# Kernel tuning notes

Hardware: AMD Instinct MI355X
Metric: run time of the kernel (lower is better)

Reference implementation:

```python
import jax, jax.numpy as jnp
import numpy as np
from functools import partial

H = 2048      # hidden_size
DI = 4096     # intermediate_size
N = 16        # ssm_state_size
K = 4         # conv_kernel_size
R = 128       # time_step_rank
B = 2
L = 1024


def setup_inputs() -> dict:
    key = jax.random.key(0)
    ks = jax.random.split(key, 10)
    s = 0.02
    return {
        "x": jax.random.normal(ks[0], (B, L, H), jnp.float32),
        "Win": jax.random.normal(ks[1], (2 * DI, H), jnp.float32) * s,      # in_proj weight
        "Wconv": jax.random.normal(ks[2], (DI, 1, K), jnp.float32) * 0.2,   # depthwise conv weight
        "bconv": jax.random.normal(ks[3], (DI,), jnp.float32) * 0.1,
        "Wx": jax.random.normal(ks[4], (R + 2 * N, DI), jnp.float32) * s,   # x_proj weight (no bias)
        "Wdt": jax.random.normal(ks[5], (DI, R), jnp.float32) * s,          # dt_proj weight
        "bdt": jax.random.normal(ks[6], (DI,), jnp.float32) * 0.1,
        "Wout": jax.random.normal(ks[7], (H, DI), jnp.float32) * s,         # out_proj weight (no bias)
        "A_log": jnp.log(jnp.broadcast_to(jnp.arange(1, N + 1, dtype=jnp.float32), (DI, N))),
        "D": jnp.ones((DI,), jnp.float32),
    }


def _silu(v):
    return v * jax.nn.sigmoid(v)


def _mamba_fwd(x, Win, Wconv, bconv, Wx, Wdt, bdt, Wout, A_log, D):
    sg = jax.lax.stop_gradient
    # in_proj -> [B, 2*DI, L]
    proj = jnp.einsum('blh,eh->bel', x, Win)
    hs, gate = proj[:, :DI], proj[:, DI:]          # [B, DI, L] each
    # depthwise causal conv1d, left pad K-1, trimmed to seq_len
    hs = jax.lax.conv_general_dilated(
        hs, Wconv, window_strides=(1,), padding=[(K - 1, 0)],
        dimension_numbers=('NCH', 'OIH', 'NCH'), feature_group_count=DI)
    hs = _silu(hs + bconv[None, :, None])          # [B, DI, L]
    # x_proj on [B, L, DI]
    ssm_p = jnp.einsum('bdl,pd->blp', hs, Wx)      # [B, L, R+2N]
    dt_in, Bm, Cm = ssm_p[..., :R], ssm_p[..., R:R + N], ssm_p[..., R + N:]
    dt = jax.nn.softplus(jnp.einsum('blr,dr->bld', dt_in, Wdt) + bdt)  # [B, L, DI]
    dt = jnp.transpose(dt, (0, 2, 1))              # [B, DI, L]
    A = -jnp.exp(A_log)                            # [DI, N]
    dA = jnp.exp(A[None, :, None, :] * dt[:, :, :, None])              # [B, DI, L, N]
    dBu = sg(dt[:, :, :, None] * Bm[:, None, :, :]) * hs[:, :, :, None]
    dA = sg(dA)
    Cm = sg(Cm)
    # sequential selective scan over time
    xs = (jnp.transpose(dA, (2, 0, 1, 3)),         # [L, B, DI, N]
          jnp.transpose(dBu, (2, 0, 1, 3)),
          jnp.transpose(Cm, (1, 0, 2)))            # [L, B, N]
    h0 = jnp.zeros((x.shape[0], DI, N), jnp.float32)

    def step(h, inp):
        dA_t, dBu_t, C_t = inp
        h = dA_t * h + dBu_t
        y = jnp.einsum('bdn,bn->bd', h, C_t)
        return h, y

    _, ys = jax.lax.scan(step, h0, xs)             # ys: [L, B, DI]
    y = jnp.transpose(ys, (1, 2, 0))               # [B, DI, L]
    y = y + hs * D[None, :, None]
    y = y * _silu(gate)
    y = y / 2.0 + sg(y / 2.0)                      # gradient-halving trick (fwd-identity)
    return jnp.einsum('bdl,hd->blh', y, Wout)      # [B, L, H]


def reference(x, Win, Wconv, bconv, Wx, Wdt, bdt, Wout, A_log, D):
    return _mamba_fwd(x, Win, Wconv, bconv, Wx, Wdt, bdt, Wout, A_log, D)
```

## Files before the change

kernel.cpp:

```cpp
#include <hip/hip_runtime.h>
#include <hip/hip_bf16.h>

#define HH 2048
#define DI 4096
#define NS 16
#define RR 128
#define NB 2
#define LL 1024
#define BL (NB*LL)
#define E2 (2*DI)
#define NPAD 256
#define NCOV 192
#define NC 16
#define CL (LL/NC)
#define KSPL 8

typedef __bf16  bf16x8 __attribute__((ext_vector_type(8)));
typedef unsigned short u16x8 __attribute__((ext_vector_type(8)));
typedef unsigned short u16x4 __attribute__((ext_vector_type(4)));
typedef float   f32x4  __attribute__((ext_vector_type(4)));
typedef _Float16 f16;
typedef _Float16 f16x4 __attribute__((ext_vector_type(4)));

__device__ __forceinline__ unsigned short f2bf(float f) {
  union { float f; unsigned u; } v; v.f = f;
  unsigned u = v.u;
  unsigned r = (u + 0x7FFFu + ((u >> 16) & 1u)) >> 16;
  return (unsigned short)r;
}
__device__ __forceinline__ float bf2f(unsigned short u) {
  union { unsigned u; float f; } v; v.u = ((unsigned)u) << 16; return v.f;
}

__device__ __forceinline__ float sigm(float x) { return 1.f / (1.f + __expf(-x)); }

__device__ __forceinline__ float softplus_hw(float v) {
  return (v > 20.f) ? v : __logf(1.f + __expf(v));
}

__device__ __forceinline__ void pow16(float q, float* w) {
  float q2 = q * q, q3 = q2 * q, q4 = q2 * q2;
  float q5 = q4 * q, q6 = q4 * q2, q7 = q4 * q3, q8 = q4 * q4;
  w[0]=q;    w[1]=q2;    w[2]=q3;    w[3]=q4;
  w[4]=q5;   w[5]=q6;    w[6]=q7;    w[7]=q8;
  w[8]=q8*q; w[9]=q8*q2; w[10]=q8*q3; w[11]=q8*q4;
  w[12]=q8*q5; w[13]=q8*q6; w[14]=q8*q7; w[15]=q8*q8;
}

__device__ __forceinline__ void gload_lds16(const void* g, void* l) {
  __builtin_amdgcn_global_load_lds(
      (const __attribute__((address_space(1))) void*)g,
      (__attribute__((address_space(3))) void*)l, 16, 0, 0);
}

#define CPRE_X    ((long)BL*HH/8)
#define CPRE_WIN  ((long)E2*HH/8)
#define CPRE_WX   ((long)NPAD*DI/8)
#define CPRE_WDT  ((long)DI*RR/8)
#define CPRE_WOUT ((long)HH*DI/8)
__global__ void cast_pre(const float* __restrict__ x, const float* __restrict__ Win,
                         const float* __restrict__ Wx, const float* __restrict__ Wdt,
                         const float* __restrict__ Wout,
                         unsigned short* __restrict__ xb, unsigned short* __restrict__ winb,
                         unsigned short* __restrict__ wxb, unsigned short* __restrict__ wdtb,
                         unsigned short* __restrict__ woutb) {
  const long NT = CPRE_X + CPRE_WIN + CPRE_WX + CPRE_WDT + CPRE_WOUT;
  long stride = (long)gridDim.x * blockDim.x;
  for (long c = (long)blockIdx.x * blockDim.x + threadIdx.x; c < NT; c += stride) {
    const float* src; unsigned short* dst; long i; bool zero = false;
    long c1 = c - CPRE_X, c2 = c1 - CPRE_WIN, c3 = c2 - CPRE_WX, c4 = c3 - CPRE_WDT;
    if (c < CPRE_X)        { src = x;    dst = xb;    i = c; }
    else if (c1 < CPRE_WIN){ src = Win;  dst = winb;  i = c1; }
    else if (c2 < CPRE_WX) { src = Wx;   dst = wxb;   i = c2; zero = (i >= 160L * (DI / 8)); }
    else if (c3 < CPRE_WDT){ src = Wdt;  dst = wdtb;  i = c3; }
    else                   { src = Wout; dst = woutb; i = c4; }
    u16x8 r;
    if (zero) {
      #pragma unroll
      for (int k = 0; k < 8; k++) r[k] = 0;
    } else {
      const float4* p = (const float4*)src + i * 2;
      float4 a = p[0], b = p[1];
      r[0]=f2bf(a.x); r[1]=f2bf(a.y); r[2]=f2bf(a.z); r[3]=f2bf(a.w);
      r[4]=f2bf(b.x); r[5]=f2bf(b.y); r[6]=f2bf(b.z); r[7]=f2bf(b.w);
    }
    ((u16x8*)dst)[i] = r;
  }
}

__global__ __launch_bounds__(256, 2) void gemm1_128(
    const unsigned short* __restrict__ A, const unsigned short* __restrict__ B,
    unsigned short* __restrict__ Chs, unsigned short* __restrict__ Cgate)
{
  __shared__ unsigned short As[128 * 32];
  __shared__ unsigned short Bs[128 * 32];

  const int tid  = threadIdx.x;
  const int lane = tid & 63;
  const int wid  = tid >> 6;
  const int mBlk = blockIdx.y * 128;
  const int nBlk = blockIdx.x * 128;
  const int wm = (wid >> 1) * 64;
  const int wn = (wid & 1) * 64;

  const int srow = wid * 32 + (lane >> 2);
  const int sk   = (lane & 3) * 8;
  const unsigned short* ga0 = A + (size_t)(mBlk + srow) * HH + sk;
  const unsigned short* ga1 = A + (size_t)(mBlk + srow + 16) * HH + sk;
  const unsigned short* gb0 = B + (size_t)(nBlk + srow) * HH + sk;
  const unsigned short* gb1 = B + (size_t)(nBlk + srow + 16) * HH + sk;
  unsigned short* la0 = &As[(wid * 32) * 32];
  unsigned short* la1 = &As[(wid * 32 + 16) * 32];
  unsigned short* lb0 = &Bs[(wid * 32) * 32];
  unsigned short* lb1 = &Bs[(wid * 32 + 16) * 32];

  const int fr = lane & 15;
  const int fq = lane >> 4;

  f32x4 acc[4][4];
  #pragma unroll
  for (int i = 0; i < 4; i++)
    #pragma unroll
    for (int j = 0; j < 4; j++) {
      acc[i][j][0] = 0.f; acc[i][j][1] = 0.f; acc[i][j][2] = 0.f; acc[i][j][3] = 0.f;
    }

  for (int k0 = 0; k0 < HH; k0 += 32) {
    __syncthreads();
    gload_lds16(ga0 + k0, la0);
    gload_lds16(ga1 + k0, la1);
    gload_lds16(gb0 + k0, lb0);
    gload_lds16(gb1 + k0, lb1);
    __syncthreads();
    bf16x8 af[4], bg[4];
    #pragma unroll
    for (int i = 0; i < 4; i++) {
      af[i] = *(const bf16x8*)&As[(wm + i * 16 + fr) * 32 + fq * 8];
      bg[i] = *(const bf16x8*)&Bs[(wn + i * 16 + fr) * 32 + fq * 8];
    }
    #pragma unroll
    for (int i = 0; i < 4; i++)
      #pragma unroll
      for (int j = 0; j < 4; j++)
        acc[i][j] = __builtin_amdgcn_mfma_f32_16x16x32_bf16(bg[j], af[i], acc[i][j], 0, 0, 0);
  }

  const int mr = lane & 15;
  const int nb = (lane >> 4) * 4;
  #pragma unroll
  for (int i = 0; i < 4; i++)
    #pragma unroll
    for (int j = 0; j < 4; j++) {
      int row = mBlk + wm + i * 16 + mr;
      int col = nBlk + wn + j * 16 + nb;
      u16x4 pk;
      #pragma unroll
      for (int r = 0; r < 4; r++) pk[r] = f2bf(acc[i][j][r]);
      if (nBlk < DI) *(u16x4*)&Chs[(size_t)row * DI + col] = pk;
      else           *(u16x4*)&Cgate[(size_t)row * DI + (col - DI)] = pk;
    }
}

__global__ __launch_bounds__(256, 2) void gemm2_splitk64(
    const unsigned short* __restrict__ A, const unsigned short* __restrict__ B,
    float* __restrict__ part)
{
  __shared__ unsigned short As[128 * 32];
  __shared__ unsigned short Bs[64 * 32];

  const int tid  = threadIdx.x;
  const int lane = tid & 63;
  const int wid  = tid >> 6;
  const int mBlk = blockIdx.y * 128;
  const int nBlk = blockIdx.x * 64;
  const int kBeg = blockIdx.z * (DI / KSPL);
  const int kEnd = kBeg + DI / KSPL;
  const int wm = (wid >> 1) * 64;
  const int wn = (wid & 1) * 32;

  const int srow = lane >> 2;
  const int sk   = (lane & 3) * 8;
  const unsigned short* ga0 = A + (size_t)(mBlk + wid * 32 + srow) * DI + sk;
  const unsigned short* ga1 = ga0 + (size_t)16 * DI;
  const unsigned short* gb  = B + (size_t)(nBlk + wid * 16 + srow) * DI + sk;
  unsigned short* la0 = &As[(wid * 32) * 32];
  unsigned short* la1 = &As[(wid * 32 + 16) * 32];
  unsigned short* lb  = &Bs[(wid * 16) * 32];

  const int fr = lane & 15;
  const int fq = lane >> 4;

  f32x4 acc[4][2];
  #pragma unroll
  for (int i = 0; i < 4; i++)
    #pragma unroll
    for (int j = 0; j < 2; j++) {
      acc[i][j][0] = 0.f; acc[i][j][1] = 0.f; acc[i][j][2] = 0.f; acc[i][j][3] = 0.f;
    }

  for (int k0 = kBeg; k0 < kEnd; k0 += 32) {
    __syncthreads();
    gload_lds16(ga0 + k0, la0);
    gload_lds16(ga1 + k0, la1);
    gload_lds16(gb  + k0, lb);
    __syncthreads();
    bf16x8 af[4], bg[2];
    #pragma unroll
    for (int i = 0; i < 4; i++)
      af[i] = *(const bf16x8*)&As[(wm + i * 16 + fr) * 32 + fq * 8];
    #pragma unroll
    for (int j = 0; j < 2; j++)
      bg[j] = *(const bf16x8*)&Bs[(wn + j * 16 + fr) * 32 + fq * 8];
    #pragma unroll
    for (int i = 0; i < 4; i++)
      #pragma unroll
      for (int j = 0; j < 2; j++)
        acc[i][j] = __builtin_amdgcn_mfma_f32_16x16x32_bf16(bg[j], af[i], acc[i][j], 0, 0, 0);
  }

  float* Cz = part + (size_t)blockIdx.z * BL * NPAD;
  const int mr = lane & 15;
  const int nb = (lane >> 4) * 4;
  #pragma unroll
  for (int i = 0; i < 4; i++)
    #pragma unroll
    for (int j = 0; j < 2; j++) {
      int row = mBlk + wm + i * 16 + mr;
      int col = nBlk + wn + j * 16 + nb;
      *(f32x4*)&Cz[(size_t)row * NPAD + col] = acc[i][j];
    }
}

__global__ __launch_bounds__(256) void reduce_ssmp(
    const float* __restrict__ part, float* __restrict__ ssmp,
    unsigned short* __restrict__ dtin)
{
  int idx = blockIdx.x * 256 + threadIdx.x;
  int row = idx / 48;
  int c4  = (idx - row * 48) * 4;
  f32x4 s = {0.f, 0.f, 0.f, 0.f};
  #pragma unroll
  for (int z = 0; z < KSPL; z++) {
    f32x4 v = *(const f32x4*)(part + (size_t)z * BL * NPAD + (size_t)row * NPAD + c4);
    s[0] += v[0]; s[1] += v[1]; s[2] += v[2]; s[3] += v[3];
  }
  *(f32x4*)(ssmp + (size_t)row * NPAD + c4) = s;
  if (c4 < RR) {
    u16x4 r;
    r[0] = f2bf(s[0]); r[1] = f2bf(s[1]); r[2] = f2bf(s[2]); r[3] = f2bf(s[3]);
    *(u16x4*)(dtin + (size_t)row * RR + c4) = r;
  }
}

__global__ __launch_bounds__(256, 2) void gemm3_dt(
    const unsigned short* __restrict__ A, const unsigned short* __restrict__ B,
    f16* __restrict__ dth, const float* __restrict__ bias)
{
  __shared__ unsigned short As[128 * 32];
  __shared__ unsigned short Bs[128 * 32];

  const int tid  = threadIdx.x;
  const int lane = tid & 63;
  const int wid  = tid >> 6;
  const int mBlk = blockIdx.y * 128;
  const int nBlk = blockIdx.x * 128;
  const int wm = (wid >> 1) * 64;
  const int wn = (wid & 1) * 64;

  const int srow = wid * 32 + (lane >> 2);
  const int sk   = (lane & 3) * 8;
  const unsigned short* ga0 = A + (size_t)(mBlk + srow) * RR + sk;
  const unsigned short* ga1 = A + (size_t)(mBlk + srow + 16) * RR + sk;
  const unsigned short* gb0 = B + (size_t)(nBlk + srow) * RR + sk;
  const unsigned short* gb1 = B + (size_t)(nBlk + srow + 16) * RR + sk;
  unsigned short* la0 = &As[(wid * 32) * 32];
  unsigned short* la1 = &As[(wid * 32 + 16) * 32];
  unsigned short* lb0 = &Bs[(wid * 32) * 32];
  unsigned short* lb1 = &Bs[(wid * 32 + 16) * 32];

  const int fr = lane & 15;
  const int fq = lane >> 4;

  f32x4 acc[4][4];
  #pragma unroll
  for (int i = 0; i < 4; i++)
    #pragma unroll
    for (int j = 0; j < 4; j++) {
      acc[i][j][0] = 0.f; acc[i][j][1] = 0.f; acc[i][j][2] = 0.f; acc[i][j][3] = 0.f;
    }

  for (int k0 = 0; k0 < RR; k0 += 32) {
    __syncthreads();
    gload_lds16(ga0 + k0, la0);
    gload_lds16(ga1 + k0, la1);
    gload_lds16(gb0 + k0, lb0);
    gload_lds16(gb1 + k0, lb1);
    __syncthreads();
    bf16x8 af[4], bg[4];
    #pragma unroll
    for (int i = 0; i < 4; i++) {
      af[i] = *(const bf16x8*)&As[(wm + i * 16 + fr) * 32 + fq * 8];
      bg[i] = *(const bf16x8*)&Bs[(wn + i * 16 + fr) * 32 + fq * 8];
    }
    #pragma unroll
    for (int i = 0; i < 4; i++)
      #pragma unroll
      for (int j = 0; j < 4; j++)
        acc[i][j] = __builtin_amdgcn_mfma_f32_16x16x32_bf16(bg[j], af[i], acc[i][j], 0, 0, 0);
  }

  const int mr = lane & 15;
  const int nb = (lane >> 4) * 4;
  #pragma unroll
  for (int i = 0; i < 4; i++)
    #pragma unroll
    for (int j = 0; j < 4; j++) {
      int row = mBlk + wm + i * 16 + mr;
      int col = nBlk + wn + j * 16 + nb;
      f32x4 bb = *(const f32x4*)&bias[col];
      f16x4 pk;
      #pragma unroll
      for (int r = 0; r < 4; r++) pk[r] = (f16)softplus_hw(acc[i][j][r] + bb[r]);
      *(f16x4*)&dth[(size_t)row * DI + col] = pk;
    }
}

__global__ __launch_bounds__(256) void conv_silu(
    const unsigned short* __restrict__ ph, const float* __restrict__ Wconv,
    const float* __restrict__ bconv, unsigned short* __restrict__ hs_b)
{
  const int d   = blockIdx.x * 256 + threadIdx.x;
  const int bl0 = blockIdx.y * 8;
  const int b   = bl0 >> 10;
  const int l0  = bl0 & 1023;
  const float w0 = Wconv[d * 4 + 0], w1 = Wconv[d * 4 + 1];
  const float w2 = Wconv[d * 4 + 2], w3 = Wconv[d * 4 + 3];
  const float bc = bconv[d];
  float in[11];
  #pragma unroll
  for (int i = 0; i < 11; i++) {
    int l = l0 - 3 + i;
    in[i] = (l < 0) ? 0.f : bf2f(ph[(size_t)(b * 1024 + l) * DI + d]);
  }
  #pragma unroll
  for (int j = 0; j < 8; j++) {
    float v = in[j] * w0 + in[j + 1] * w1 + in[j + 2] * w2 + in[j + 3] * w3 + bc;
    v = v * sigm(v);
    hs_b[(size_t)(bl0 + j) * DI + d] = f2bf(v);
  }
}

template<int PASS>
__global__ __launch_bounds__(256) void scan_chunk(
    const float* __restrict__ ssm_p, const f16* __restrict__ dth,
    const unsigned short* __restrict__ hs_b, const unsigned short* __restrict__ gate_b,
    const float* __restrict__ Dv,
    f16* __restrict__ summ, const f16* __restrict__ h0buf,
    unsigned short* __restrict__ y_b)
{
  const int d = blockIdx.x * 256 + threadIdx.x;
  const int c = blockIdx.y;
  const int b = blockIdx.z;
  const float Dd = Dv[d];
  float h[16];
  float sdt = 0.f;
  if (PASS == 0) {
    #pragma unroll
    for (int n = 0; n < 16; n++) h[n] = 0.f;
  } else {
    #pragma unroll
    for (int n = 0; n < 16; n++)
      h[n] = (float)h0buf[((size_t)(b * NC + c) * 16 + n) * DI + d];
  }
  const float* sp = ssm_p + ((size_t)b * LL + c * CL) * NPAD;
  const size_t bl0 = (size_t)b * LL + c * CL;
  for (int l = 0; l < CL; ++l) {
    size_t bl = bl0 + l;
    float dt = (float)dth[bl * DI + d];
    float hs = bf2f(hs_b[bl * DI + d]);
    float u = dt * hs;
    float q = __expf(-dt);
    float w[16];
    pow16(q, w);
    float y = 0.f;
    #pragma unroll
    for (int n = 0; n < 16; n++) {
      float Bn = sp[l * NPAD + 128 + n];
      h[n] = w[n] * h[n] + u * Bn;
      if (PASS == 1) y += h[n] * sp[l * NPAD + 144 + n];
    }
    if (PASS == 0) sdt += dt;
    if (PASS == 1) {
      float gate = bf2f(gate_b[bl * DI + d]);
      float yy = (y + hs * Dd) * gate * sigm(gate);
      y_b[bl * DI + d] = f2bf(yy);
    }
  }
  if (PASS == 0) {
    float p = __expf(-sdt);
    float pw[16];
    pow16(p, pw);
    #pragma unroll
    for (int n = 0; n < 16; n++) {
      summ[((size_t)(b * NC + c) * 32 + n)      * DI + d] = (f16)pw[n];
      summ[((size_t)(b * NC + c) * 32 + 16 + n) * DI + d] = (f16)h[n];
    }
  }
}

__global__ __launch_bounds__(256) void scan_combine(
    const f16* __restrict__ summ, f16* __restrict__ h0buf)
{
  int idx = blockIdx.x * 256 + threadIdx.x;
  int d = idx & (DI - 1);
  int rest = idx >> 12;
  int n = rest & 15;
  int b = rest >> 4;
  float h = 0.f;
  for (int c = 0; c < NC; c++) {
    h0buf[((size_t)(b * NC + c) * 16 + n) * DI + d] = (f16)h;
    float Pv = (float)summ[((size_t)(b * NC + c) * 32 + n)      * DI + d];
    float Hv = (float)summ[((size_t)(b * NC + c) * 32 + 16 + n) * DI + d];
    h = Pv * h + Hv;
  }
}

__global__ __launch_bounds__(256, 2) void gemm_nt_64(
    const unsigned short* __restrict__ A, const unsigned short* __restrict__ B,
    float* __restrict__ C, int K, int lda, int ldb, int ldc)
{
  __shared__ unsigned short As[128 * 32];
  __shared__ unsigned short Bs[64 * 32];

  const int tid  = threadIdx.x;
  const int lane = tid & 63;
  const int wid  = tid >> 6;
  const int mBlk = blockIdx.y * 128;
  const int nBlk = blockIdx.x * 64;
  const int wm = (wid >> 1) * 64;
  const int wn = (wid & 1) * 32;

  const int srow = lane >> 2;
  const int sk   = (lane & 3) * 8;
  const unsigned short* ga0 = A + (size_t)(mBlk + wid * 32 + srow) * lda + sk;
  const unsigned short* ga1 = ga0 + (size_t)16 * lda;
  const unsigned short* gb  = B + (size_t)(nBlk + wid * 16 + srow) * ldb + sk;
  unsigned short* la0 = &As[(wid * 32) * 32];
  unsigned short* la1 = &As[(wid * 32 + 16) * 32];
  unsigned short* lb  = &Bs[(wid * 16) * 32];

  const int fr = lane & 15;
  const int fq = lane >> 4;

  f32x4 acc[4][2];
  #pragma unroll
  for (int i = 0; i < 4; i++)
    #pragma unroll
    for (int j = 0; j < 2; j++) {
      acc[i][j][0] = 0.f; acc[i][j][1] = 0.f; acc[i][j][2] = 0.f; acc[i][j][3] = 0.f;
    }

  for (int k0 = 0; k0 < K; k0 += 32) {
    __syncthreads();
    gload_lds16(ga0 + k0, la0);
    gload_lds16(ga1 + k0, la1);
    gload_lds16(gb  + k0, lb);
    __syncthreads();
    bf16x8 af[4], bg[2];
    #pragma unroll
    for (int i = 0; i < 4; i++)
      af[i] = *(const bf16x8*)&As[(wm + i * 16 + fr) * 32 + fq * 8];
    #pragma unroll
    for (int j = 0; j < 2; j++)
      bg[j] = *(const bf16x8*)&Bs[(wn + j * 16 + fr) * 32 + fq * 8];
    #pragma unroll
    for (int i = 0; i < 4; i++)
      #pragma unroll
      for (int j = 0; j < 2; j++)
        acc[i][j] = __builtin_amdgcn_mfma_f32_16x16x32_bf16(bg[j], af[i], acc[i][j], 0, 0, 0);
  }

  const int mr = lane & 15;
  const int nb = (lane >> 4) * 4;
  #pragma unroll
  for (int i = 0; i < 4; i++)
    #pragma unroll
    for (int j = 0; j < 2; j++) {
      int row = mBlk + wm + i * 16 + mr;
      int col = nBlk + wn + j * 16 + nb;
      *(f32x4*)&C[(size_t)row * ldc + col] = acc[i][j];
    }
}

extern "C" void kernel_launch(void* const* d_in, const int* in_sizes, int n_in,
                              void* d_out, int out_size, void* d_ws, size_t ws_size,
                              hipStream_t stream) {
  const float* x     = (const float*)d_in[0];
  const float* Win   = (const float*)d_in[1];
  const float* Wconv = (const float*)d_in[2];
  const float* bconv = (const float*)d_in[3];
  const float* Wx    = (const float*)d_in[4];
  const float* Wdt   = (const float*)d_in[5];
  const float* bdt   = (const float*)d_in[6];
  const float* Wout  = (const float*)d_in[7];
  const float* Dv    = (const float*)d_in[9];
  float* out = (float*)d_out;

  char* ws = (char*)d_ws;
  size_t o = 0;
  auto take = [&](size_t sz) { char* p = ws + o; o += (sz + 255) & ~(size_t)255; return p; };

  unsigned short* ph_b   = (unsigned short*)take((size_t)BL * DI * 2);
  unsigned short* gate_b = (unsigned short*)take((size_t)BL * DI * 2);
  unsigned short* hs_b   = (unsigned short*)take((size_t)BL * DI * 2);
  float*          ssmp   = (float*)         take((size_t)BL * NPAD * 4);
  unsigned short* dtin   = (unsigned short*)take((size_t)BL * RR * 2);
  f16*            dth    = (f16*)           take((size_t)BL * DI * 2);
  unsigned short* wxb    = (unsigned short*)take((size_t)NPAD * DI * 2);
  unsigned short* wdtb   = (unsigned short*)take((size_t)DI * RR * 2);
  unsigned short* woutb  = (unsigned short*)take((size_t)HH * DI * 2);
  char*           summ_r = take((size_t)KSPL * BL * NPAD * 4);
  f16*            h0b    = (f16*)           take((size_t)NB * NC * 16 * DI * 2);
  char* uni = take((size_t)BL * HH * 2 + (size_t)E2 * HH * 2);
  unsigned short* xb    = (unsigned short*)uni;
  unsigned short* winb  = (unsigned short*)(uni + (size_t)BL * HH * 2);
  unsigned short* y_b   = (unsigned short*)uni;
  float* part = (float*)summ_r;
  f16*   summ = (f16*)summ_r;

  hipLaunchKernelGGL(cast_pre, dim3(2048), dim3(256), 0, stream,
                     x, Win, Wx, Wdt, Wout, xb, winb, wxb, wdtb, woutb);

  hipLaunchKernelGGL(gemm1_128, dim3(E2 / 128, BL / 128), dim3(256), 0, stream,
                     xb, winb, ph_b, gate_b);

  hipLaunchKernelGGL(conv_silu, dim3(DI / 256, BL / 8), dim3(256), 0, stream,
                     ph_b, Wconv, bconv, hs_b);

  hipLaunchKernelGGL(gemm2_splitk64, dim3(NCOV / 64, BL / 128, KSPL), dim3(256), 0, stream,
                     hs_b, wxb, part);
  hipLaunchKernelGGL(reduce_ssmp, dim3(BL * 48 / 256), dim3(256), 0, stream,
                     part, ssmp, dtin);

  hipLaunchKernelGGL(gemm3_dt, dim3(DI / 128, BL / 128), dim3(256), 0, stream,
                     dtin, wdtb, dth, bdt);

  hipLaunchKernelGGL((scan_chunk<0>), dim3(DI / 256, NC, NB), dim3(256), 0, stream,
                     ssmp, dth, hs_b, gate_b, Dv, summ, h0b, y_b);
  hipLaunchKernelGGL(scan_combine, dim3(NB * NS * DI / 256), dim3(256), 0, stream, summ, h0b);
  hipLaunchKernelGGL((scan_chunk<1>), dim3(DI / 256, NC, NB), dim3(256), 0, stream,
                     ssmp, dth, hs_b, gate_b, Dv, summ, h0b, y_b);

  hipLaunchKernelGGL(gemm_nt_64, dim3(HH / 64, BL / 128), dim3(256), 0, stream,
                     y_b, woutb, out, DI, DI, DI, HH);
}
```

Baseline: 280.1 us.

## Double GEMM K-tile to 64 with XOR-swizzled LDS and fold scan combine into pass 1

The three bf16 GEMMs now stage 64-wide K tiles in LDS using an XOR swizzle on 8-element groups. This halves the number of barrier-separated iterations and is meant to avoid LDS bank conflicts on the fragment reads. The separate scan_combine kernel and its h0 buffer are removed. Each pass-1 scan chunk now recomputes its initial state by serially combining the summaries of all preceding chunks, which trades one launch and a buffer round-trip for redundant loads in later chunks. The split-K and out_proj GEMMs are unified into one templated kernel.

```diff
diff --git a/kernel.cpp b/kernel.cpp
--- a/kernel.cpp
+++ b/kernel.cpp
@@ -92,8 +92,8 @@
     const unsigned short* __restrict__ A, const unsigned short* __restrict__ B,
     unsigned short* __restrict__ Chs, unsigned short* __restrict__ Cgate)
 {
-  __shared__ unsigned short As[128 * 32];
-  __shared__ unsigned short Bs[128 * 32];
+  __shared__ unsigned short As[128 * 64];
+  __shared__ unsigned short Bs[128 * 64];
 
   const int tid  = threadIdx.x;
   const int lane = tid & 63;
@@ -103,19 +103,16 @@
   const int wm = (wid >> 1) * 64;
   const int wn = (wid & 1) * 64;
 
-  const int srow = wid * 32 + (lane >> 2);
-  const int sk   = (lane & 3) * 8;
-  const unsigned short* ga0 = A + (size_t)(mBlk + srow) * HH + sk;
-  const unsigned short* ga1 = A + (size_t)(mBlk + srow + 16) * HH + sk;
-  const unsigned short* gb0 = B + (size_t)(nBlk + srow) * HH + sk;
-  const unsigned short* gb1 = B + (size_t)(nBlk + srow + 16) * HH + sk;
-  unsigned short* la0 = &As[(wid * 32) * 32];
-  unsigned short* la1 = &As[(wid * 32 + 16) * 32];
-  unsigned short* lb0 = &Bs[(wid * 32) * 32];
-  unsigned short* lb1 = &Bs[(wid * 32 + 16) * 32];
+  const int srow = tid >> 3;
+  const int sq   = (tid & 7) ^ (srow & 7);
+  const unsigned short* gA = A + (size_t)(mBlk + srow) * HH + sq * 8;
+  const unsigned short* gB = B + (size_t)(nBlk + srow) * HH + sq * 8;
+  unsigned short* lA = &As[srow * 64 + (tid & 7) * 8];
+  unsigned short* lB = &Bs[srow * 64 + (tid & 7) * 8];
 
   const int fr = lane & 15;
   const int fq = lane >> 4;
+  const int sx = fr & 7;
 
   f32x4 acc[4][4];
   #pragma unroll
@@ -125,24 +122,29 @@
       acc[i][j][0] = 0.f; acc[i][j][1] = 0.f; acc[i][j][2] = 0.f; acc[i][j][3] = 0.f;
     }
 
-  for (int k0 = 0; k0 < HH; k0 += 32) {
-    __syncthreads();
-    gload_lds16(ga0 + k0, la0);
-    gload_lds16(ga1 + k0, la1);
-    gload_lds16(gb0 + k0, lb0);
-    gload_lds16(gb1 + k0, lb1);
-    __syncthreads();
-    bf16x8 af[4], bg[4];
-    #pragma unroll
-    for (int i = 0; i < 4; i++) {
-      af[i] = *(const bf16x8*)&As[(wm + i * 16 + fr) * 32 + fq * 8];
-      bg[i] = *(const bf16x8*)&Bs[(wn + i * 16 + fr) * 32 + fq * 8];
-    }
-    #pragma unroll
-    for (int i = 0; i < 4; i++)
+  for (int k0 = 0; k0 < HH; k0 += 64) {
+    __syncthreads();
+    #pragma unroll
+    for (int g = 0; g < 4; g++) {
+      gload_lds16(gA + (size_t)(g * 32) * HH + k0, lA + g * 32 * 64);
+      gload_lds16(gB + (size_t)(g * 32) * HH + k0, lB + g * 32 * 64);
+    }
+    __syncthreads();
+    #pragma unroll
+    for (int h = 0; h < 2; h++) {
+      bf16x8 af[4], bg[4];
+      #pragma unroll
+      for (int i = 0; i < 4; i++)
+        af[i] = *(const bf16x8*)&As[(wm + i * 16 + fr) * 64 + ((h * 4 + fq) ^ sx) * 8];
       #pragma unroll
       for (int j = 0; j < 4; j++)
-        acc[i][j] = __builtin_amdgcn_mfma_f32_16x16x32_bf16(bg[j], af[i], acc[i][j], 0, 0, 0);
+        bg[j] = *(const bf16x8*)&Bs[(wn + j * 16 + fr) * 64 + ((h * 4 + fq) ^ sx) * 8];
+      #pragma unroll
+      for (int i = 0; i < 4; i++)
+        #pragma unroll
+        for (int j = 0; j < 4; j++)
+          acc[i][j] = __builtin_amdgcn_mfma_f32_16x16x32_bf16(bg[j], af[i], acc[i][j], 0, 0, 0);
+    }
   }
 
   const int mr = lane & 15;
@@ -161,34 +163,38 @@
     }
 }
 
-__global__ __launch_bounds__(256, 2) void gemm2_splitk64(
+template<int SPLITK>
+__global__ __launch_bounds__(256, 2) void gemm_nt_12864(
     const unsigned short* __restrict__ A, const unsigned short* __restrict__ B,
-    float* __restrict__ part)
-{
-  __shared__ unsigned short As[128 * 32];
-  __shared__ unsigned short Bs[64 * 32];
+    float* __restrict__ C, int K, int lda, int ldb, int ldc)
+{
+  __shared__ unsigned short As[128 * 64];
+  __shared__ unsigned short Bs[64 * 64];
 
   const int tid  = threadIdx.x;
   const int lane = tid & 63;
   const int wid  = tid >> 6;
   const int mBlk = blockIdx.y * 128;
   const int nBlk = blockIdx.x * 64;
-  const int kBeg = blockIdx.z * (DI / KSPL);
-  const int kEnd = kBeg + DI / KSPL;
+  int kBeg = 0, kEnd = K;
+  if (SPLITK) {
+    kBeg = blockIdx.z * (K / KSPL);
+    kEnd = kBeg + K / KSPL;
+    C += (size_t)blockIdx.z * BL * NPAD;
+  }
   const int wm = (wid >> 1) * 64;
   const int wn = (wid & 1) * 32;
 
-  const int srow = lane >> 2;
-  const int sk   = (lane & 3) * 8;
-  const unsigned short* ga0 = A + (size_t)(mBlk + wid * 32 + srow) * DI + sk;
-  const unsigned short* ga1 = ga0 + (size_t)16 * DI;
-  const unsigned short* gb  = B + (size_t)(nBlk + wid * 16 + srow) * DI + sk;
-  unsigned short* la0 = &As[(wid * 32) * 32];
-  unsigned short* la1 = &As[(wid * 32 + 16) * 32];
-  unsigned short* lb  = &Bs[(wid * 16) * 32];
+  const int srow = tid >> 3;
+  const int sq   = (tid & 7) ^ (srow & 7);
+  const unsigned short* gA = A + (size_t)(mBlk + srow) * lda + sq * 8;
+  const unsigned short* gB = B + (size_t)(nBlk + srow) * ldb + sq * 8;
+  unsigned short* lA = &As[srow * 64 + (tid & 7) * 8];
+  unsigned short* lB = &Bs[srow * 64 + (tid & 7) * 8];
 
   const int fr = lane & 15;
   const int fq = lane >> 4;
+  const int sx = fr & 7;
 
   f32x4 acc[4][2];
   #pragma unroll
@@ -198,27 +204,32 @@
       acc[i][j][0] = 0.f; acc[i][j][1] = 0.f; acc[i][j][2] = 0.f; acc[i][j][3] = 0.f;
     }
 
-  for (int k0 = kBeg; k0 < kEnd; k0 += 32) {
-    __syncthreads();
-    gload_lds16(ga0 + k0, la0);
-    gload_lds16(ga1 + k0, la1);
-    gload_lds16(gb  + k0, lb);
-    __syncthreads();
-    bf16x8 af[4], bg[2];
-    #pragma unroll
-    for (int i = 0; i < 4; i++)
-      af[i] = *(const bf16x8*)&As[(wm + i * 16 + fr) * 32 + fq * 8];
-    #pragma unroll
-    for (int j = 0; j < 2; j++)
-      bg[j] = *(const bf16x8*)&Bs[(wn + j * 16 + fr) * 32 + fq * 8];
-    #pragma unroll
-    for (int i = 0; i < 4; i++)
+  for (int k0 = kBeg; k0 < kEnd; k0 += 64) {
+    __syncthreads();
+    #pragma unroll
+    for (int g = 0; g < 4; g++)
+      gload_lds16(gA + (size_t)(g * 32) * lda + k0, lA + g * 32 * 64);
+    #pragma unroll
+    for (int g = 0; g < 2; g++)
+      gload_lds16(gB + (size_t)(g * 32) * ldb + k0, lB + g * 32 * 64);
+    __syncthreads();
+    #pragma unroll
+    for (int h = 0; h < 2; h++) {
+      bf16x8 af[4], bg[2];
+      #pragma unroll
+      for (int i = 0; i < 4; i++)
+        af[i] = *(const bf16x8*)&As[(wm + i * 16 + fr) * 64 + ((h * 4 + fq) ^ sx) * 8];
       #pragma unroll
       for (int j = 0; j < 2; j++)
-        acc[i][j] = __builtin_amdgcn_mfma_f32_16x16x32_bf16(bg[j], af[i], acc[i][j], 0, 0, 0);
-  }
-
-  float* Cz = part + (size_t)blockIdx.z * BL * NPAD;
+        bg[j] = *(const bf16x8*)&Bs[(wn + j * 16 + fr) * 64 + ((h * 4 + fq) ^ sx) * 8];
+      #pragma unroll
+      for (int i = 0; i < 4; i++)
+        #pragma unroll
+        for (int j = 0; j < 2; j++)
+          acc[i][j] = __builtin_amdgcn_mfma_f32_16x16x32_bf16(bg[j], af[i], acc[i][j], 0, 0, 0);
+    }
+  }
+
   const int mr = lane & 15;
   const int nb = (lane >> 4) * 4;
   #pragma unroll
@@ -227,7 +238,7 @@
     for (int j = 0; j < 2; j++) {
       int row = mBlk + wm + i * 16 + mr;
       int col = nBlk + wn + j * 16 + nb;
-      *(f32x4*)&Cz[(size_t)row * NPAD + col] = acc[i][j];
+      *(f32x4*)&C[(size_t)row * ldc + col] = acc[i][j];
     }
 }
 
@@ -355,8 +366,7 @@
     const float* __restrict__ ssm_p, const f16* __restrict__ dth,
     const unsigned short* __restrict__ hs_b, const unsigned short* __restrict__ gate_b,
     const float* __restrict__ Dv,
-    f16* __restrict__ summ, const f16* __restrict__ h0buf,
-    unsigned short* __restrict__ y_b)
+    f16* __restrict__ summ, unsigned short* __restrict__ y_b)
 {
   const int d = blockIdx.x * 256 + threadIdx.x;
   const int c = blockIdx.y;
@@ -364,13 +374,18 @@
   const float Dd = Dv[d];
   float h[16];
   float sdt = 0.f;
-  if (PASS == 0) {
-    #pragma unroll
-    for (int n = 0; n < 16; n++) h[n] = 0.f;
-  } else {
-    #pragma unroll
-    for (int n = 0; n < 16; n++)
-      h[n] = (float)h0buf[((size_t)(b * NC + c) * 16 + n) * DI + d];
+  #pragma unroll
+  for (int n = 0; n < 16; n++) h[n] = 0.f;
+  if (PASS == 1) {
+    for (int cc = 0; cc < c; cc++) {
+      const f16* sP = summ + ((size_t)(b * NC + cc) * 32) * DI + d;
+      #pragma unroll
+      for (int n = 0; n < 16; n++) {
+        float Pv = (float)sP[(size_t)n * DI];
+        float Hv = (float)sP[(size_t)(16 + n) * DI];
+        h[n] = Pv * h[n] + Hv;
+      }
+    }
   }
   const float* sp = ssm_p + ((size_t)b * LL + c * CL) * NPAD;
   const size_t bl0 = (size_t)b * LL + c * CL;
@@ -406,90 +421,6 @@
       summ[((size_t)(b * NC + c) * 32 + 16 + n) * DI + d] = (f16)h[n];
     }
   }
-}
-
-__global__ __launch_bounds__(256) void scan_combine(
-    const f16* __restrict__ summ, f16* __restrict__ h0buf)
-{
-  int idx = blockIdx.x * 256 + threadIdx.x;
-  int d = idx & (DI - 1);
-  int rest = idx >> 12;
-  int n = rest & 15;
-  int b = rest >> 4;
-  float h = 0.f;
-  for (int c = 0; c < NC; c++) {
-    h0buf[((size_t)(b * NC + c) * 16 + n) * DI + d] = (f16)h;
-    float Pv = (float)summ[((size_t)(b * NC + c) * 32 + n)      * DI + d];
-    float Hv = (float)summ[((size_t)(b * NC + c) * 32 + 16 + n) * DI + d];
-    h = Pv * h + Hv;
-  }
-}
-
-__global__ __launch_bounds__(256, 2) void gemm_nt_64(
-    const unsigned short* __restrict__ A, const unsigned short* __restrict__ B,
-    float* __restrict__ C, int K, int lda, int ldb, int ldc)
-{
-  __shared__ unsigned short As[128 * 32];
-  __shared__ unsigned short Bs[64 * 32];
-
-  const int tid  = threadIdx.x;
-  const int lane = tid & 63;
-  const int wid  = tid >> 6;
-  const int mBlk = blockIdx.y * 128;
-  const int nBlk = blockIdx.x * 64;
-  const int wm = (wid >> 1) * 64;
-  const int wn = (wid & 1) * 32;
-
-  const int srow = lane >> 2;
-  const int sk   = (lane & 3) * 8;
-  const unsigned short* ga0 = A + (size_t)(mBlk + wid * 32 + srow) * lda + sk;
-  const unsigned short* ga1 = ga0 + (size_t)16 * lda;
-  const unsigned short* gb  = B + (size_t)(nBlk + wid * 16 + srow) * ldb + sk;
-  unsigned short* la0 = &As[(wid * 32) * 32];
-  unsigned short* la1 = &As[(wid * 32 + 16) * 32];
-  unsigned short* lb  = &Bs[(wid * 16) * 32];
-
-  const int fr = lane & 15;
-  const int fq = lane >> 4;
-
-  f32x4 acc[4][2];
-  #pragma unroll
-  for (int i = 0; i < 4; i++)
-    #pragma unroll
-    for (int j = 0; j < 2; j++) {
-      acc[i][j][0] = 0.f; acc[i][j][1] = 0.f; acc[i][j][2] = 0.f; acc[i][j][3] = 0.f;
-    }
-
-  for (int k0 = 0; k0 < K; k0 += 32) {
-    __syncthreads();
-    gload_lds16(ga0 + k0, la0);
-    gload_lds16(ga1 + k0, la1);
-    gload_lds16(gb  + k0, lb);
-    __syncthreads();
-    bf16x8 af[4], bg[2];
-    #pragma unroll
-    for (int i = 0; i < 4; i++)
-      af[i] = *(const bf16x8*)&As[(wm + i * 16 + fr) * 32 + fq * 8];
-    #pragma unroll
-    for (int j = 0; j < 2; j++)
-      bg[j] = *(const bf16x8*)&Bs[(wn + j * 16 + fr) * 32 + fq * 8];
-    #pragma unroll
-    for (int i = 0; i < 4; i++)
-      #pragma unroll
-      for (int j = 0; j < 2; j++)
-        acc[i][j] = __builtin_amdgcn_mfma_f32_16x16x32_bf16(bg[j], af[i], acc[i][j], 0, 0, 0);
-  }
-
-  const int mr = lane & 15;
-  const int nb = (lane >> 4) * 4;
-  #pragma unroll
-  for (int i = 0; i < 4; i++)
-    #pragma unroll
-    for (int j = 0; j < 2; j++) {
-      int row = mBlk + wm + i * 16 + mr;
-      int col = nBlk + wn + j * 16 + nb;
-      *(f32x4*)&C[(size_t)row * ldc + col] = acc[i][j];
-    }
 }
 
 extern "C" void kernel_launch(void* const* d_in, const int* in_sizes, int n_in,
@@ -520,7 +451,6 @@
   unsigned short* wdtb   = (unsigned short*)take((size_t)DI * RR * 2);
   unsigned short* woutb  = (unsigned short*)take((size_t)HH * DI * 2);
   char*           summ_r = take((size_t)KSPL * BL * NPAD * 4);
-  f16*            h0b    = (f16*)           take((size_t)NB * NC * 16 * DI * 2);
   char* uni = take((size_t)BL * HH * 2 + (size_t)E2 * HH * 2);
   unsigned short* xb    = (unsigned short*)uni;
   unsigned short* winb  = (unsigned short*)(uni + (size_t)BL * HH * 2);
@@ -537,8 +467,8 @@
   hipLaunchKernelGGL(conv_silu, dim3(DI / 256, BL / 8), dim3(256), 0, stream,
                      ph_b, Wconv, bconv, hs_b);
 
-  hipLaunchKernelGGL(gemm2_splitk64, dim3(NCOV / 64, BL / 128, KSPL), dim3(256), 0, stream,
-                     hs_b, wxb, part);
+  hipLaunchKernelGGL((gemm_nt_12864<1>), dim3(NCOV / 64, BL / 128, KSPL), dim3(256), 0, stream,
+                     hs_b, wxb, part, DI, DI, DI, NPAD);
   hipLaunchKernelGGL(reduce_ssmp, dim3(BL * 48 / 256), dim3(256), 0, stream,
                      part, ssmp, dtin);
 
@@ -546,11 +476,10 @@
                      dtin, wdtb, dth, bdt);
 
   hipLaunchKernelGGL((scan_chunk<0>), dim3(DI / 256, NC, NB), dim3(256), 0, stream,
-                     ssmp, dth, hs_b, gate_b, Dv, summ, h0b, y_b);
-  hipLaunchKernelGGL(scan_combine, dim3(NB * NS * DI / 256), dim3(256), 0, stream, summ, h0b);
+                     ssmp, dth, hs_b, gate_b, Dv, summ, y_b);
   hipLaunchKernelGGL((scan_chunk<1>), dim3(DI / 256, NC, NB), dim3(256), 0, stream,
-                     ssmp, dth, hs_b, gate_b, Dv, summ, h0b, y_b);
-
-  hipLaunchKernelGGL(gemm_nt_64, dim3(HH / 64, BL / 128), dim3(256), 0, stream,
+                     ssmp, dth, hs_b, gate_b, Dv, summ, y_b);
+
+  hipLaunchKernelGGL((gemm_nt_12864<0>), dim3(HH / 64, BL / 128), dim3(256), 0, stream,
                      y_b, woutb, out, DI, DI, DI, HH);
 }
```

New measurement: 266.7 us. 4.8% less time.
